# Optimization experiments

Measured on AMD Instinct MI355X. Metric: run time of the kernel, lower is better.

Reference implementation:

```python
import jax, jax.numpy as jnp
import numpy as np

BLANK = 0
B, T, U = 4, 128, 64
EPROJS, EMBED, DUNITS, JOINT, ODIM = 512, 512, 1024, 512, 2048


def lstm_cell(x, h, c, W_ih, W_hh, b_ih, b_hh):
    # PyTorch LSTMCell: gates ordered (i, f, g, o)
    gates = x @ W_ih.T + b_ih + h @ W_hh.T + b_hh
    i, f, g, o = jnp.split(gates, 4, axis=-1)
    c_new = jax.nn.sigmoid(f) * c + jax.nn.sigmoid(i) * jnp.tanh(g)
    h_new = jax.nn.sigmoid(o) * jnp.tanh(c_new)
    return h_new, c_new


def setup_inputs() -> dict:
    key = jax.random.key(0)
    ks = jax.random.split(key, 20)
    s = 0.05
    embed = jax.random.normal(ks[2], (ODIM, EMBED)) * s
    embed = embed.at[BLANK].set(0.0)  # padding_idx
    return {
        'hs_pad': jax.random.normal(ks[0], (B, T, EPROJS)),
        'ys_in_pad': jax.random.randint(ks[1], (B, U), 0, ODIM, dtype=jnp.int32),
        'embed': embed,
        'W_ih0': jax.random.normal(ks[3], (4 * DUNITS, EMBED)) * s,
        'W_hh0': jax.random.normal(ks[4], (4 * DUNITS, DUNITS)) * s,
        'b_ih0': jax.random.normal(ks[5], (4 * DUNITS,)) * s,
        'b_hh0': jax.random.normal(ks[6], (4 * DUNITS,)) * s,
        'W_ih1': jax.random.normal(ks[7], (4 * DUNITS, DUNITS)) * s,
        'W_hh1': jax.random.normal(ks[8], (4 * DUNITS, DUNITS)) * s,
        'b_ih1': jax.random.normal(ks[9], (4 * DUNITS,)) * s,
        'b_hh1': jax.random.normal(ks[10], (4 * DUNITS,)) * s,
        'W_enc': jax.random.normal(ks[11], (JOINT, EPROJS)) * s,
        'b_enc': jax.random.normal(ks[12], (JOINT,)) * s,
        'W_dec': jax.random.normal(ks[13], (JOINT, DUNITS)) * s,
        'W_out': jax.random.normal(ks[14], (ODIM, JOINT)) * s,
        'b_out': jax.random.normal(ks[15], (ODIM,)) * s,
    }


def reference(hs_pad, ys_in_pad, embed, W_ih0, W_hh0, b_ih0, b_hh0,
              W_ih1, W_hh1, b_ih1, b_hh1, W_enc, b_enc, W_dec, W_out, b_out):
    # Embedding with padding_idx=blank (blank row contributes zero).
    eys = embed[ys_in_pad] * (ys_in_pad != BLANK)[..., None].astype(embed.dtype)  # (B,U,E)

    def step(carry, ey):
        h0, c0, h1, c1 = carry
        h0, c0 = lstm_cell(ey, h0, c0, W_ih0, W_hh0, b_ih0, b_hh0)
        h1, c1 = lstm_cell(h0, h1, c1, W_ih1, W_hh1, b_ih1, b_hh1)
        return (h0, c0, h1, c1), h1

    z0 = jnp.zeros((hs_pad.shape[0], DUNITS), hs_pad.dtype)
    _, hs = jax.lax.scan(step, (z0, z0, z0, z0), jnp.swapaxes(eys, 0, 1))
    h_dec = jnp.swapaxes(hs, 0, 1)  # (B,U,Hdec)

    # Joint network: broadcast-add + tanh + output projection.
    enc_p = jnp.einsum('bte,je->btj', hs_pad, W_enc) + b_enc   # (B,T,J)
    dec_p = jnp.einsum('bud,jd->buj', h_dec, W_dec)            # (B,U,J)
    z = jnp.tanh(enc_p[:, :, None, :] + dec_p[:, None, :, :])  # (B,T,U,J)
    return jnp.einsum('btuj,oj->btuo', z, W_out) + b_out       # (B,T,U,odim)
```

## Files before the change

kernel.cpp:

```cpp
#include <hip/hip_runtime.h>
#include <stdint.h>

typedef short bf16x8 __attribute__((ext_vector_type(8)));
typedef float f32x4 __attribute__((ext_vector_type(4)));
typedef unsigned int u32x4 __attribute__((ext_vector_type(4)));

__device__ __forceinline__ unsigned short f2bf(float f) {
  union { float f; unsigned int i; } v; v.f = f;
  unsigned int r = v.i + 0x7FFF + ((v.i >> 16) & 1);
  return (unsigned short)(r >> 16);
}
__device__ __forceinline__ float bfu2f(unsigned short u) {
  union { unsigned int i; float f; } v; v.i = ((unsigned int)u) << 16; return v.f;
}
__device__ __forceinline__ void gload_lds16(const void* g, void* l) {
  __builtin_amdgcn_global_load_lds(
      (const __attribute__((address_space(1))) unsigned int*)g,
      (__attribute__((address_space(3))) unsigned int*)l,
      16, 0, 0);
}
__device__ __forceinline__ void store16_coh(unsigned int* p, u32x4 v) {
  asm volatile("global_store_dwordx4 %0, %1, off sc0 sc1" :: "v"(p), "v"(v) : "memory");
}
__device__ __forceinline__ void spin_load6(const unsigned int* p0, const unsigned int* p1,
                                           const unsigned int* p2, const unsigned int* p3,
                                           const unsigned int* p4, const unsigned int* p5,
                                           u32x4& r0, u32x4& r1, u32x4& r2,
                                           u32x4& r3, u32x4& r4, u32x4& r5) {
  asm volatile(
      "global_load_dwordx4 %0, %6, off sc0 sc1\n\t"
      "global_load_dwordx4 %1, %7, off sc0 sc1\n\t"
      "global_load_dwordx4 %2, %8, off sc0 sc1\n\t"
      "global_load_dwordx4 %3, %9, off sc0 sc1\n\t"
      "global_load_dwordx4 %4, %10, off sc0 sc1\n\t"
      "global_load_dwordx4 %5, %11, off sc0 sc1\n\t"
      "s_waitcnt vmcnt(0)"
      : "=&v"(r0), "=&v"(r1), "=&v"(r2), "=&v"(r3), "=&v"(r4), "=&v"(r5)
      : "v"(p0), "v"(p1), "v"(p2), "v"(p3), "v"(p4), "v"(p5)
      : "memory");
}
__device__ __forceinline__ void spin_load3p(const unsigned int* p0, const unsigned int* p1,
                                            const unsigned int* p2, const unsigned int* pp,
                                            u32x4& r0, u32x4& r1, u32x4& r2, unsigned int& pt) {
  asm volatile(
      "global_load_dwordx4 %0, %4, off sc0 sc1\n\t"
      "global_load_dwordx4 %1, %5, off sc0 sc1\n\t"
      "global_load_dwordx4 %2, %6, off sc0 sc1\n\t"
      "global_load_dword %3, %7, off sc0 sc1\n\t"
      "s_waitcnt vmcnt(0)"
      : "=&v"(r0), "=&v"(r1), "=&v"(r2), "=&v"(pt)
      : "v"(p0), "v"(p1), "v"(p2), "v"(pp)
      : "memory");
}

__global__ __launch_bounds__(256) void k_cvt(const float* __restrict__ s0, const float* __restrict__ s1,
                                             const float* __restrict__ s2, const float* __restrict__ s3,
                                             unsigned short* __restrict__ d0, unsigned short* __restrict__ d1,
                                             unsigned short* __restrict__ d2, unsigned short* __restrict__ d3) {
  int j = blockIdx.x * 256 + threadIdx.x;
  const float* s; unsigned short* d; int o;
  if (j < 524288)       { s = s0; d = d0; o = j; }
  else if (j < 1048576) { s = s1; d = d1; o = j - 524288; }
  else if (j < 1572864) { s = s2; d = d2; o = j - 1048576; }
  else                  { s = s3; d = d3; o = j - 1572864; }
  size_t off = (size_t)o * 8;
  f32x4 v0 = *(const f32x4*)(s + off);
  f32x4 v1 = *(const f32x4*)(s + off + 4);
  bf16x8 r;
#pragma unroll
  for (int k = 0; k < 4; k++) { r[k] = (short)f2bf(v0[k]); r[4 + k] = (short)f2bf(v1[k]); }
  *(bf16x8*)(d + off) = r;
}

__global__ __launch_bounds__(256) void k_prep(const int* __restrict__ ys,
                                              const float* __restrict__ embed,
                                              float* __restrict__ eys,
                                              unsigned int* __restrict__ exch) {
  int idx = blockIdx.x * 256 + threadIdx.x;
  int row = idx >> 6;
  int e = (idx & 63) * 8;
  int y = ys[row];
  f32x4 v0 = {0.f, 0.f, 0.f, 0.f}, v1 = {0.f, 0.f, 0.f, 0.f};
  if (y != 0) {
    v0 = *(const f32x4*)(embed + (size_t)y * 512 + e);
    v1 = *(const f32x4*)(embed + (size_t)y * 512 + e + 4);
  }
  *(f32x4*)(eys + (size_t)row * 512 + e) = v0;
  *(f32x4*)(eys + (size_t)row * 512 + e + 4) = v1;
  exch[idx] = 0u;
  exch[idx + 16384] = 0u;
}

__global__ __launch_bounds__(256) void k_gemm_bias(const float* __restrict__ A,
                                                   const float* __restrict__ W,
                                                   const float* __restrict__ b1,
                                                   const float* __restrict__ b2,
                                                   void* __restrict__ Cout, int obf,
                                                   int M, int N, int K) {
  __shared__ unsigned short Als[64][40];
  __shared__ unsigned short Wls[64][40];
  int tid = threadIdx.x;
  int lane = tid & 63, wid = tid >> 6;
  int mtiles = M >> 6;
  int mt = blockIdx.x % mtiles, nt = blockIdx.x / mtiles;
  int srow = tid >> 2, sseg = tid & 3;
  f32x4 acc[4];
#pragma unroll
  for (int nf = 0; nf < 4; nf++) acc[nf] = (f32x4){0.f, 0.f, 0.f, 0.f};

  for (int kc = 0; kc < K; kc += 32) {
    const float* ap = A + (size_t)(mt * 64 + srow) * K + kc + sseg * 8;
    const float* wp = W + (size_t)(nt * 64 + srow) * K + kc + sseg * 8;
    f32x4 a0 = *(const f32x4*)ap, a1 = *(const f32x4*)(ap + 4);
    f32x4 w0 = *(const f32x4*)wp, w1 = *(const f32x4*)(wp + 4);
    bf16x8 av, wv;
#pragma unroll
    for (int k = 0; k < 4; k++) {
      av[k] = (short)f2bf(a0[k]); av[4 + k] = (short)f2bf(a1[k]);
      wv[k] = (short)f2bf(w0[k]); wv[4 + k] = (short)f2bf(w1[k]);
    }
    __syncthreads();
    *(bf16x8*)(&Als[srow][sseg * 8]) = av;
    *(bf16x8*)(&Wls[srow][sseg * 8]) = wv;
    __syncthreads();
    bf16x8 af = *(const bf16x8*)(&Als[wid * 16 + (lane & 15)][(lane >> 4) * 8]);
#pragma unroll
    for (int nf = 0; nf < 4; nf++) {
      bf16x8 bf = *(const bf16x8*)(&Wls[nf * 16 + (lane & 15)][(lane >> 4) * 8]);
      acc[nf] = __builtin_amdgcn_mfma_f32_16x16x32_bf16(af, bf, acc[nf], 0, 0, 0);
    }
  }
  int rloc = (lane >> 4) * 4;
  int col0 = lane & 15;
#pragma unroll
  for (int nf = 0; nf < 4; nf++) {
    int n = nt * 64 + nf * 16 + col0;
    float bias = 0.f;
    if (b1) bias += b1[n];
    if (b2) bias += b2[n];
#pragma unroll
    for (int r = 0; r < 4; r++) {
      int m = mt * 64 + wid * 16 + rloc + r;
      float v = acc[nf][r] + bias;
      if (obf) ((unsigned short*)Cout)[(size_t)m * N + n] = f2bf(v);
      else     ((float*)Cout)[(size_t)m * N + n] = v;
    }
  }
}

__global__ __launch_bounds__(512) void k_lstm_fused(
    const float* __restrict__ X0,
    float* __restrict__ hdec,
    const unsigned short* __restrict__ W_hh0,
    const unsigned short* __restrict__ W_ih1,
    const unsigned short* __restrict__ W_hh1,
    const float* __restrict__ b_ih1,
    const float* __restrict__ b_hh1,
    unsigned int* __restrict__ exch) {
  __shared__ unsigned short X_lds[4][2064];
  __shared__ float red[8][4][16][4];
  int tid = threadIdx.x;
  int lane = tid & 63, w = tid >> 6;
  bool isL1 = blockIdx.x >= 64;
  int bidl = blockIdx.x & 63;
  int base = bidl * 16;
  unsigned int* REC0 = exch;
  unsigned int* REC1 = exch + 16384;

  bf16x8 wf[4][8];
  int ch = lane & 15;
  int klo = (lane >> 4) << 3;
  int kb = isL1 ? w * 256 : w * 128;
#pragma unroll
  for (int nt = 0; nt < 4; nt++) {
    int grow = nt * 1024 + base + ch;
    if (!isL1) {
#pragma unroll
      for (int ks = 0; ks < 4; ks++)
        wf[nt][ks] = *(const bf16x8*)(W_hh0 + (size_t)grow * 1024 + kb + ks * 32 + klo);
    } else {
#pragma unroll
      for (int ks = 0; ks < 8; ks++) {
        int k = kb + ks * 32 + klo;
        const unsigned short* src = (k < 1024) ? (W_ih1 + (size_t)grow * 1024 + k)
                                               : (W_hh1 + (size_t)grow * 1024 + (k - 1024));
        wf[nt][ks] = *(const bf16x8*)src;
      }
    }
  }

  float creg = 0.f;
  float bs0 = 0.f, bs1 = 0.f, bs2 = 0.f, bs3 = 0.f;
  int gch = tid >> 2, gb = tid & 3;
  if (isL1 && tid < 64) {
    int c = base + gch;
    bs0 = b_ih1[c] + b_hh1[c];
    bs1 = b_ih1[1024 + c] + b_hh1[1024 + c];
    bs2 = b_ih1[2048 + c] + b_hh1[2048 + c];
    bs3 = b_ih1[3072 + c] + b_hh1[3072 + c];
  }

  int uoff[3], upb[3], us[3]; bool uneed[3];
#pragma unroll
  for (int r = 0; r < 3; r++) {
    int u = tid + r * 512;
    uneed[r] = (u < 1408);
    int uc = uneed[r] ? u : 1407;
    int pb = uc / 22;
    int s = uc - pb * 22;
    upb[r] = pb; us[r] = s;
    uoff[r] = pb * 128 + s * 4;
  }

#define STAGE_UNIT(rv, rr, off1024)                                           \
  if (uneed[rv]) {                                                            \
    int pb_ = upb[rv], s_ = us[rv];                                           \
    _Pragma("unroll")                                                         \
    for (int j_ = 0; j_ < 3; j_++) {                                          \
      int i_ = 3 * s_ + j_;                                                   \
      if (i_ < 64) {                                                          \
        union { unsigned int u; float f; } cv_; cv_.u = rr[j_];               \
        X_lds[i_ & 3][off1024 + pb_ * 16 + (i_ >> 2)] = f2bf(cv_.f);          \
      }                                                                       \
    }                                                                         \
  }

  int ar = ch & 3;
  if (!isL1) {
    for (int p = 0; p < 64; p++) {
      float xp0 = 0.f, xp1 = 0.f, xp2 = 0.f, xp3 = 0.f;
      if (tid < 64) {
        const float* x0p = X0 + ((size_t)(gb * 64 + p)) * 4096 + base + gch;
        xp0 = x0p[0]; xp1 = x0p[1024]; xp2 = x0p[2048]; xp3 = x0p[3072];
      }
      {
        unsigned int* b0 = REC0 + (unsigned)(p & 1) * 8192;
        const unsigned int* pp = REC1 + (unsigned)((p - 1) & 1) * 8192 + (tid & 63) * 128 + 3;
        unsigned expP = (p == 0) ? 0u : (unsigned)(p - 1);
        u32x4 r0, r1, r2; unsigned int pt;
        while (true) {
          spin_load3p(b0 + uoff[0], b0 + uoff[1], b0 + uoff[2], pp, r0, r1, r2, pt);
          bool ok = (!uneed[0] || r0[3] == (unsigned)p) && (!uneed[1] || r1[3] == (unsigned)p) &&
                    (!uneed[2] || r2[3] == (unsigned)p) && (pt >= expP);
          if (ok) break;
          __builtin_amdgcn_s_sleep(1);
        }
        STAGE_UNIT(0, r0, 0) STAGE_UNIT(1, r1, 0) STAGE_UNIT(2, r2, 0)
      }
      __syncthreads();
      {
        f32x4 acc[4];
#pragma unroll
        for (int nt = 0; nt < 4; nt++) acc[nt] = (f32x4){0.f, 0.f, 0.f, 0.f};
#pragma unroll
        for (int ks = 0; ks < 4; ks++) {
          bf16x8 a = *(const bf16x8*)&X_lds[ar][kb + ks * 32 + klo];
#pragma unroll
          for (int nt = 0; nt < 4; nt++)
            acc[nt] = __builtin_amdgcn_mfma_f32_16x16x32_bf16(a, wf[nt][ks], acc[nt], 0, 0, 0);
        }
        if (lane < 16) {
#pragma unroll
          for (int nt = 0; nt < 4; nt++) *(f32x4*)&red[w][nt][lane][0] = acc[nt];
        }
      }
      __syncthreads();
      if (tid < 64) {
        float g0 = 0.f, g1 = 0.f, g2 = 0.f, g3 = 0.f;
#pragma unroll
        for (int w8 = 0; w8 < 8; w8++) {
          g0 += red[w8][0][gch][gb]; g1 += red[w8][1][gch][gb];
          g2 += red[w8][2][gch][gb]; g3 += red[w8][3][gch][gb];
        }
        g0 += xp0; g1 += xp1; g2 += xp2; g3 += xp3;
        float ii = 1.f / (1.f + __expf(-g0));
        float ff = 1.f / (1.f + __expf(-g1));
        float oo = 1.f / (1.f + __expf(-g3));
        float cn = ff * creg + ii * tanhf(g2);
        creg = cn;
        float hn = oo * tanhf(cn);
        int l = tid;
        float v0 = __shfl(hn, 3 * l);
        float v1 = __shfl(hn, 3 * l + 1);
        float v2 = __shfl(hn, 3 * l + 2);
        if (l < 22) {
          unsigned tag = (unsigned)(p + 1);
          unsigned int* rec = REC0 + (tag & 1) * 8192 + bidl * 128 + l * 4;
          u32x4 d;
          d[0] = __float_as_uint(v0); d[1] = __float_as_uint(v1);
          d[2] = __float_as_uint(v2); d[3] = tag;
          store16_coh(rec, d);
        }
      }
    }
  } else {
    for (int p = 1; p <= 64; p++) {
      {
        unsigned int* b0 = REC0 + (unsigned)(p & 1) * 8192;
        unsigned int* b1 = REC1 + (unsigned)((p - 1) & 1) * 8192;
        u32x4 r0, r1, r2, r3, r4, r5;
        unsigned exp0 = (unsigned)p, exp1 = (unsigned)(p - 1);
        while (true) {
          spin_load6(b0 + uoff[0], b0 + uoff[1], b0 + uoff[2],
                     b1 + uoff[0], b1 + uoff[1], b1 + uoff[2],
                     r0, r1, r2, r3, r4, r5);
          bool ok = (!uneed[0] || (r0[3] == exp0 && r3[3] == exp1)) &&
                    (!uneed[1] || (r1[3] == exp0 && r4[3] == exp1)) &&
                    (!uneed[2] || (r2[3] == exp0 && r5[3] == exp1));
          if (ok) break;
          __builtin_amdgcn_s_sleep(1);
        }
        STAGE_UNIT(0, r0, 0) STAGE_UNIT(1, r1, 0) STAGE_UNIT(2, r2, 0)
        STAGE_UNIT(0, r3, 1024) STAGE_UNIT(1, r4, 1024) STAGE_UNIT(2, r5, 1024)
      }
      __syncthreads();
      {
        f32x4 acc[4];
#pragma unroll
        for (int nt = 0; nt < 4; nt++) acc[nt] = (f32x4){0.f, 0.f, 0.f, 0.f};
#pragma unroll
        for (int ks = 0; ks < 8; ks++) {
          bf16x8 a = *(const bf16x8*)&X_lds[ar][kb + ks * 32 + klo];
#pragma unroll
          for (int nt = 0; nt < 4; nt++)
            acc[nt] = __builtin_amdgcn_mfma_f32_16x16x32_bf16(a, wf[nt][ks], acc[nt], 0, 0, 0);
        }
        if (lane < 16) {
#pragma unroll
          for (int nt = 0; nt < 4; nt++) *(f32x4*)&red[w][nt][lane][0] = acc[nt];
        }
      }
      __syncthreads();
      if (tid < 64) {
        float g0 = 0.f, g1 = 0.f, g2 = 0.f, g3 = 0.f;
#pragma unroll
        for (int w8 = 0; w8 < 8; w8++) {
          g0 += red[w8][0][gch][gb]; g1 += red[w8][1][gch][gb];
          g2 += red[w8][2][gch][gb]; g3 += red[w8][3][gch][gb];
        }
        g0 += bs0; g1 += bs1; g2 += bs2; g3 += bs3;
        float ii = 1.f / (1.f + __expf(-g0));
        float ff = 1.f / (1.f + __expf(-g1));
        float oo = 1.f / (1.f + __expf(-g3));
        float cn = ff * creg + ii * tanhf(g2);
        creg = cn;
        float hn = oo * tanhf(cn);
        hdec[((size_t)(gb * 64 + (p - 1))) * 1024 + base + gch] = hn;
        int l = tid;
        float v0 = __shfl(hn, 3 * l);
        float v1 = __shfl(hn, 3 * l + 1);
        float v2 = __shfl(hn, 3 * l + 2);
        if (l < 22) {
          unsigned tag = (unsigned)p;
          unsigned int* rec = REC1 + (tag & 1) * 8192 + bidl * 128 + l * 4;
          u32x4 d;
          d[0] = __float_as_uint(v0); d[1] = __float_as_uint(v1);
          d[2] = __float_as_uint(v2); d[3] = tag;
          store16_coh(rec, d);
        }
      }
    }
  }
#undef STAGE_UNIT
}

__global__ __launch_bounds__(256) void k_z(const unsigned short* __restrict__ encpb,
                                           const unsigned short* __restrict__ decpb,
                                           unsigned short* __restrict__ Z) {
  int idx = blockIdx.x * 256 + threadIdx.x;
  int m = idx >> 6;
  int k0 = (idx & 63) * 8;
  int bt = m >> 6;
  int b = m >> 13, u = m & 63;
  bf16x8 ev = *(const bf16x8*)(encpb + (size_t)bt * 512 + k0);
  bf16x8 dv = *(const bf16x8*)(decpb + (size_t)(b * 64 + u) * 512 + k0);
  bf16x8 r;
#pragma unroll
  for (int j = 0; j < 8; j++) {
    float x = bfu2f((unsigned short)ev[j]) + bfu2f((unsigned short)dv[j]);
    float e = __expf(x + x);
    r[j] = (short)f2bf(1.f - 2.f / (e + 1.f));
  }
  *(bf16x8*)(Z + (size_t)m * 512 + k0) = r;
}

__global__ __launch_bounds__(512, 2) void k_gemm_out(const unsigned short* __restrict__ Z,
                                                     const unsigned short* __restrict__ Wout,
                                                     const float* __restrict__ bout,
                                                     float* __restrict__ out) {
  __shared__ unsigned short Wls[8][8192];
  int tid = threadIdx.x;
  int lane = tid & 63, wid = tid >> 6;
  int bid = blockIdx.x;
  int mpart = bid & 15, ngroup = bid >> 4;

#pragma unroll
  for (int kc = 0; kc < 8; kc++) {
    unsigned short* dst = &Wls[kc][0];
#pragma unroll
    for (int q = 0; q < 2; q++) {
      int idx = tid + q * 512;
      int n = idx >> 3, sl = idx & 7;
      int ss = sl ^ (n & 7);
      gload_lds16(Wout + (size_t)(ngroup * 128 + n) * 512 + kc * 64 + ss * 8, dst + idx * 8);
    }
  }
  float bb[8];
#pragma unroll
  for (int nf = 0; nf < 8; nf++) bb[nf] = bout[ngroup * 128 + nf * 16 + (lane & 15)];
  asm volatile("s_waitcnt vmcnt(0)" ::: "memory");
  __syncthreads();

  int rowwave = mpart * 2048 + wid * 256;
  int ocol0 = ngroup * 128;
  for (int mg = 0; mg < 4; mg++) {
    int rowbase = rowwave + mg * 64;
    f32x4 acc[4][8];
#pragma unroll
    for (int mf = 0; mf < 4; mf++)
#pragma unroll
      for (int nf = 0; nf < 8; nf++) acc[mf][nf] = (f32x4){0.f, 0.f, 0.f, 0.f};

#pragma unroll
    for (int ks = 0; ks < 16; ks++) {
      bf16x8 a[4];
#pragma unroll
      for (int mf = 0; mf < 4; mf++) {
        int r = rowbase + mf * 16 + (lane & 15);
        a[mf] = *(const bf16x8*)(Z + (size_t)r * 512 + ks * 32 + ((lane >> 4) << 3));
      }
      const unsigned short* Wb = &Wls[ks >> 1][0];
      int slot = (ks & 1) * 4 + (lane >> 4);
#pragma unroll
      for (int nf = 0; nf < 8; nf++) {
        int nl = nf * 16 + (lane & 15);
        int phys = slot ^ (nl & 7);
        bf16x8 bfr = *(const bf16x8*)(Wb + nl * 64 + phys * 8);
#pragma unroll
        for (int mf = 0; mf < 4; mf++)
          acc[mf][nf] = __builtin_amdgcn_mfma_f32_16x16x32_bf16(a[mf], bfr, acc[mf][nf], 0, 0, 0);
      }
    }
#pragma unroll
    for (int mf = 0; mf < 4; mf++) {
      int rb = rowbase + mf * 16 + ((lane >> 4) << 2);
#pragma unroll
      for (int nf = 0; nf < 8; nf++) {
        int o = ocol0 + nf * 16 + (lane & 15);
        float bias = bb[nf];
#pragma unroll
        for (int q = 0; q < 4; q++)
          __builtin_nontemporal_store(acc[mf][nf][q] + bias, &out[(size_t)(rb + q) * 2048 + o]);
      }
    }
  }
}

extern "C" void kernel_launch(void* const* d_in, const int* in_sizes, int n_in,
                              void* d_out, int out_size, void* d_ws, size_t ws_size,
                              hipStream_t stream) {
  const float* hs   = (const float*)d_in[0];
  const int*   ys   = (const int*)d_in[1];
  const float* emb  = (const float*)d_in[2];
  const float* Wih0 = (const float*)d_in[3];
  const float* Whh0 = (const float*)d_in[4];
  const float* bih0 = (const float*)d_in[5];
  const float* bhh0 = (const float*)d_in[6];
  const float* Wih1 = (const float*)d_in[7];
  const float* Whh1 = (const float*)d_in[8];
  const float* bih1 = (const float*)d_in[9];
  const float* bhh1 = (const float*)d_in[10];
  const float* Wenc = (const float*)d_in[11];
  const float* benc = (const float*)d_in[12];
  const float* Wdec = (const float*)d_in[13];
  const float* Wout = (const float*)d_in[14];
  const float* bout = (const float*)d_in[15];

  char* ws = (char*)d_ws;
  unsigned short* Woutb = (unsigned short*)(ws + 0);
  unsigned short* encpb = (unsigned short*)(ws + 2097152);
  unsigned short* decpb = (unsigned short*)(ws + 2621440);
  unsigned int*   exch  = (unsigned int*)(ws + 2883584);
  unsigned short* Z     = (unsigned short*)(ws + 3031040);
  float*          eys   = (float*)(ws + 3031040);
  float*          X0    = (float*)(ws + 3555328);
  float*          hdec  = (float*)(ws + 7749632);
  unsigned short* Whh0b = (unsigned short*)(ws + 8798208);
  unsigned short* Wih1b = (unsigned short*)(ws + 17186816);
  unsigned short* Whh1b = (unsigned short*)(ws + 25575424);
  float*          out   = (float*)d_out;

  k_cvt<<<6656, 256, 0, stream>>>(Whh0, Wih1, Whh1, Wout, Whh0b, Wih1b, Whh1b, Woutb);
  k_prep<<<64, 256, 0, stream>>>(ys, emb, eys, exch);
  k_gemm_bias<<<256, 256, 0, stream>>>(eys, Wih0, bih0, bhh0, X0, 0, 256, 4096, 512);
  k_gemm_bias<<<64, 256, 0, stream>>>(hs, Wenc, benc, nullptr, encpb, 1, 512, 512, 512);
  k_lstm_fused<<<128, 512, 0, stream>>>(X0, hdec, Whh0b, Wih1b, Whh1b, bih1, bhh1, exch);
  k_gemm_bias<<<32, 256, 0, stream>>>(hdec, Wdec, nullptr, nullptr, decpb, 1, 256, 512, 1024);
  k_z<<<8192, 256, 0, stream>>>(encpb, decpb, Z);
  k_gemm_out<<<256, 512, 0, stream>>>(Z, Woutb, bout, out);
}
```

Before: 421.9 us.

## Fuse LSTM, decoder projection and joint GEMM into one persistent pipelined kernel

Merges the recurrent LSTM, the decoder projection, the tanh joint and the output GEMM into a single 256-block kernel. Decoder-projection blocks spin on the layer-1 hidden-state exchange and publish per-step tags. Joint blocks wait on those tags and compute each decoder step's output slice as soon as it is ready, building tanh(enc+dec) on the fly instead of materialising Z. The aim is to hide the joint GEMM behind the serial LSTM and remove the Z write/read and extra launches. This relies on all blocks being co-resident for the spin-waits and changes the output write order to a per-u stride.

```diff
diff --git a/kernel.cpp b/kernel.cpp
--- a/kernel.cpp
+++ b/kernel.cpp
@@ -55,14 +55,17 @@
 
 __global__ __launch_bounds__(256) void k_cvt(const float* __restrict__ s0, const float* __restrict__ s1,
                                              const float* __restrict__ s2, const float* __restrict__ s3,
+                                             const float* __restrict__ s4,
                                              unsigned short* __restrict__ d0, unsigned short* __restrict__ d1,
-                                             unsigned short* __restrict__ d2, unsigned short* __restrict__ d3) {
+                                             unsigned short* __restrict__ d2, unsigned short* __restrict__ d3,
+                                             unsigned short* __restrict__ d4) {
   int j = blockIdx.x * 256 + threadIdx.x;
   const float* s; unsigned short* d; int o;
   if (j < 524288)       { s = s0; d = d0; o = j; }
   else if (j < 1048576) { s = s1; d = d1; o = j - 524288; }
   else if (j < 1572864) { s = s2; d = d2; o = j - 1048576; }
-  else                  { s = s3; d = d3; o = j - 1572864; }
+  else if (j < 1703936) { s = s3; d = d3; o = j - 1572864; }
+  else                  { s = s4; d = d4; o = j - 1703936; }
   size_t off = (size_t)o * 8;
   f32x4 v0 = *(const f32x4*)(s + off);
   f32x4 v1 = *(const f32x4*)(s + off + 4);
@@ -75,7 +78,8 @@
 __global__ __launch_bounds__(256) void k_prep(const int* __restrict__ ys,
                                               const float* __restrict__ embed,
                                               float* __restrict__ eys,
-                                              unsigned int* __restrict__ exch) {
+                                              unsigned int* __restrict__ exch,
+                                              unsigned int* __restrict__ dtag) {
   int idx = blockIdx.x * 256 + threadIdx.x;
   int row = idx >> 6;
   int e = (idx & 63) * 8;
@@ -89,6 +93,7 @@
   *(f32x4*)(eys + (size_t)row * 512 + e + 4) = v1;
   exch[idx] = 0u;
   exch[idx + 16384] = 0u;
+  if (idx < 1024) dtag[idx] = 0u;
 }
 
 __global__ __launch_bounds__(256) void k_gemm_bias(const float* __restrict__ A,
@@ -148,100 +153,264 @@
   }
 }
 
-__global__ __launch_bounds__(512) void k_lstm_fused(
+__global__ __launch_bounds__(512) void k_mega(
     const float* __restrict__ X0,
-    float* __restrict__ hdec,
     const unsigned short* __restrict__ W_hh0,
     const unsigned short* __restrict__ W_ih1,
     const unsigned short* __restrict__ W_hh1,
     const float* __restrict__ b_ih1,
     const float* __restrict__ b_hh1,
-    unsigned int* __restrict__ exch) {
-  __shared__ unsigned short X_lds[4][2064];
-  __shared__ float red[8][4][16][4];
+    unsigned int* __restrict__ exch,
+    const unsigned short* __restrict__ Wdecb,
+    float* __restrict__ decpf,
+    unsigned int* __restrict__ dtag,
+    const unsigned short* __restrict__ encpb,
+    const unsigned short* __restrict__ Woutb,
+    const float* __restrict__ bout,
+    float* __restrict__ out) {
+  __shared__ unsigned long long smem[16384];
   int tid = threadIdx.x;
   int lane = tid & 63, w = tid >> 6;
-  bool isL1 = blockIdx.x >= 64;
-  int bidl = blockIdx.x & 63;
-  int base = bidl * 16;
+  int bid = blockIdx.x;
   unsigned int* REC0 = exch;
   unsigned int* REC1 = exch + 16384;
 
-  bf16x8 wf[4][8];
-  int ch = lane & 15;
-  int klo = (lane >> 4) << 3;
-  int kb = isL1 ? w * 256 : w * 128;
-#pragma unroll
-  for (int nt = 0; nt < 4; nt++) {
-    int grow = nt * 1024 + base + ch;
+  if (bid < 128) {
+    unsigned short (*X_lds)[2064] = (unsigned short (*)[2064])smem;
+    float (*red)[4][16][4] = (float (*)[4][16][4])((char*)smem + 16512);
+    bool isL1 = bid >= 64;
+    int bidl = bid & 63;
+    int base = bidl * 16;
+
+    bf16x8 wf[4][8];
+    int ch = lane & 15;
+    int klo = (lane >> 4) << 3;
+    int kb = isL1 ? w * 256 : w * 128;
+#pragma unroll
+    for (int nt = 0; nt < 4; nt++) {
+      int grow = nt * 1024 + base + ch;
+      if (!isL1) {
+#pragma unroll
+        for (int ks = 0; ks < 4; ks++)
+          wf[nt][ks] = *(const bf16x8*)(W_hh0 + (size_t)grow * 1024 + kb + ks * 32 + klo);
+      } else {
+#pragma unroll
+        for (int ks = 0; ks < 8; ks++) {
+          int k = kb + ks * 32 + klo;
+          const unsigned short* src = (k < 1024) ? (W_ih1 + (size_t)grow * 1024 + k)
+                                                 : (W_hh1 + (size_t)grow * 1024 + (k - 1024));
+          wf[nt][ks] = *(const bf16x8*)src;
+        }
+      }
+    }
+
+    float creg = 0.f;
+    float bs0 = 0.f, bs1 = 0.f, bs2 = 0.f, bs3 = 0.f;
+    int gch = tid >> 2, gb = tid & 3;
+    if (isL1 && tid < 64) {
+      int c = base + gch;
+      bs0 = b_ih1[c] + b_hh1[c];
+      bs1 = b_ih1[1024 + c] + b_hh1[1024 + c];
+      bs2 = b_ih1[2048 + c] + b_hh1[2048 + c];
+      bs3 = b_ih1[3072 + c] + b_hh1[3072 + c];
+    }
+
+    int uoff[3], upb[3], us[3]; bool uneed[3];
+#pragma unroll
+    for (int r = 0; r < 3; r++) {
+      int u = tid + r * 512;
+      uneed[r] = (u < 1408);
+      int uc = uneed[r] ? u : 1407;
+      int pb = uc / 22;
+      int s = uc - pb * 22;
+      upb[r] = pb; us[r] = s;
+      uoff[r] = pb * 128 + s * 4;
+    }
+
+#define STAGE_UNIT(rv, rr, off1024)                                           \
+    if (uneed[rv]) {                                                          \
+      int pb_ = upb[rv], s_ = us[rv];                                         \
+      _Pragma("unroll")                                                       \
+      for (int j_ = 0; j_ < 3; j_++) {                                        \
+        int i_ = 3 * s_ + j_;                                                 \
+        if (i_ < 64) {                                                        \
+          union { unsigned int u; float f; } cv_; cv_.u = rr[j_];             \
+          X_lds[i_ & 3][off1024 + pb_ * 16 + (i_ >> 2)] = f2bf(cv_.f);        \
+        }                                                                     \
+      }                                                                       \
+    }
+
+    int ar = ch & 3;
     if (!isL1) {
+      for (int p = 0; p < 64; p++) {
+        float xp0 = 0.f, xp1 = 0.f, xp2 = 0.f, xp3 = 0.f;
+        if (tid < 64) {
+          const float* x0p = X0 + ((size_t)(gb * 64 + p)) * 4096 + base + gch;
+          xp0 = x0p[0]; xp1 = x0p[1024]; xp2 = x0p[2048]; xp3 = x0p[3072];
+        }
+        {
+          unsigned int* b0 = REC0 + (unsigned)(p & 1) * 8192;
+          const unsigned int* pp = REC1 + (unsigned)((p - 1) & 1) * 8192 + (tid & 63) * 128 + 3;
+          unsigned expP = (p == 0) ? 0u : (unsigned)(p - 1);
+          u32x4 r0, r1, r2; unsigned int pt;
+          while (true) {
+            spin_load3p(b0 + uoff[0], b0 + uoff[1], b0 + uoff[2], pp, r0, r1, r2, pt);
+            bool ok = (!uneed[0] || r0[3] == (unsigned)p) && (!uneed[1] || r1[3] == (unsigned)p) &&
+                      (!uneed[2] || r2[3] == (unsigned)p) && (pt >= expP);
+            if (ok) break;
+            __builtin_amdgcn_s_sleep(1);
+          }
+          STAGE_UNIT(0, r0, 0) STAGE_UNIT(1, r1, 0) STAGE_UNIT(2, r2, 0)
+        }
+        __syncthreads();
+        {
+          f32x4 acc[4];
+#pragma unroll
+          for (int nt = 0; nt < 4; nt++) acc[nt] = (f32x4){0.f, 0.f, 0.f, 0.f};
+#pragma unroll
+          for (int ks = 0; ks < 4; ks++) {
+            bf16x8 a = *(const bf16x8*)&X_lds[ar][kb + ks * 32 + klo];
+#pragma unroll
+            for (int nt = 0; nt < 4; nt++)
+              acc[nt] = __builtin_amdgcn_mfma_f32_16x16x32_bf16(a, wf[nt][ks], acc[nt], 0, 0, 0);
+          }
+          if (lane < 16) {
+#pragma unroll
+            for (int nt = 0; nt < 4; nt++) *(f32x4*)&red[w][nt][lane][0] = acc[nt];
+          }
+        }
+        __syncthreads();
+        if (tid < 64) {
+          float g0 = 0.f, g1 = 0.f, g2 = 0.f, g3 = 0.f;
+#pragma unroll
+          for (int w8 = 0; w8 < 8; w8++) {
+            g0 += red[w8][0][gch][gb]; g1 += red[w8][1][gch][gb];
+            g2 += red[w8][2][gch][gb]; g3 += red[w8][3][gch][gb];
+          }
+          g0 += xp0; g1 += xp1; g2 += xp2; g3 += xp3;
+          float ii = 1.f / (1.f + __expf(-g0));
+          float ff = 1.f / (1.f + __expf(-g1));
+          float oo = 1.f / (1.f + __expf(-g3));
+          float cn = ff * creg + ii * tanhf(g2);
+          creg = cn;
+          float hn = oo * tanhf(cn);
+          int l = tid;
+          float v0 = __shfl(hn, 3 * l);
+          float v1 = __shfl(hn, 3 * l + 1);
+          float v2 = __shfl(hn, 3 * l + 2);
+          if (l < 22) {
+            unsigned tag = (unsigned)(p + 1);
+            unsigned int* rec = REC0 + (tag & 1) * 8192 + bidl * 128 + l * 4;
+            u32x4 d;
+            d[0] = __float_as_uint(v0); d[1] = __float_as_uint(v1);
+            d[2] = __float_as_uint(v2); d[3] = tag;
+            store16_coh(rec, d);
+          }
+        }
+      }
+    } else {
+      for (int p = 1; p <= 64; p++) {
+        {
+          unsigned int* b0 = REC0 + (unsigned)(p & 1) * 8192;
+          unsigned int* b1 = REC1 + (unsigned)((p - 1) & 1) * 8192;
+          u32x4 r0, r1, r2, r3, r4, r5;
+          unsigned exp0 = (unsigned)p, exp1 = (unsigned)(p - 1);
+          while (true) {
+            spin_load6(b0 + uoff[0], b0 + uoff[1], b0 + uoff[2],
+                       b1 + uoff[0], b1 + uoff[1], b1 + uoff[2],
+                       r0, r1, r2, r3, r4, r5);
+            bool ok = (!uneed[0] || (r0[3] == exp0 && r3[3] == exp1)) &&
+                      (!uneed[1] || (r1[3] == exp0 && r4[3] == exp1)) &&
+                      (!uneed[2] || (r2[3] == exp0 && r5[3] == exp1));
+            if (ok) break;
+            __builtin_amdgcn_s_sleep(1);
+          }
+          STAGE_UNIT(0, r0, 0) STAGE_UNIT(1, r1, 0) STAGE_UNIT(2, r2, 0)
+          STAGE_UNIT(0, r3, 1024) STAGE_UNIT(1, r4, 1024) STAGE_UNIT(2, r5, 1024)
+        }
+        __syncthreads();
+        {
+          f32x4 acc[4];
+#pragma unroll
+          for (int nt = 0; nt < 4; nt++) acc[nt] = (f32x4){0.f, 0.f, 0.f, 0.f};
+#pragma unroll
+          for (int ks = 0; ks < 8; ks++) {
+            bf16x8 a = *(const bf16x8*)&X_lds[ar][kb + ks * 32 + klo];
+#pragma unroll
+            for (int nt = 0; nt < 4; nt++)
+              acc[nt] = __builtin_amdgcn_mfma_f32_16x16x32_bf16(a, wf[nt][ks], acc[nt], 0, 0, 0);
+          }
+          if (lane < 16) {
+#pragma unroll
+            for (int nt = 0; nt < 4; nt++) *(f32x4*)&red[w][nt][lane][0] = acc[nt];
+          }
+        }
+        __syncthreads();
+        if (tid < 64) {
+          float g0 = 0.f, g1 = 0.f, g2 = 0.f, g3 = 0.f;
+#pragma unroll
+          for (int w8 = 0; w8 < 8; w8++) {
+            g0 += red[w8][0][gch][gb]; g1 += red[w8][1][gch][gb];
+            g2 += red[w8][2][gch][gb]; g3 += red[w8][3][gch][gb];
+          }
+          g0 += bs0; g1 += bs1; g2 += bs2; g3 += bs3;
+          float ii = 1.f / (1.f + __expf(-g0));
+          float ff = 1.f / (1.f + __expf(-g1));
+          float oo = 1.f / (1.f + __expf(-g3));
+          float cn = ff * creg + ii * tanhf(g2);
+          creg = cn;
+          float hn = oo * tanhf(cn);
+          int l = tid;
+          float v0 = __shfl(hn, 3 * l);
+          float v1 = __shfl(hn, 3 * l + 1);
+          float v2 = __shfl(hn, 3 * l + 2);
+          if (l < 22) {
+            unsigned tag = (unsigned)p;
+            unsigned int* rec = REC1 + (tag & 1) * 8192 + bidl * 128 + l * 4;
+            u32x4 d;
+            d[0] = __float_as_uint(v0); d[1] = __float_as_uint(v1);
+            d[2] = __float_as_uint(v2); d[3] = tag;
+            store16_coh(rec, d);
+          }
+        }
+      }
+    }
+  } else if (bid < 144) {
+    unsigned short (*X_lds)[2064] = (unsigned short (*)[2064])smem;
+    float (*red)[4][16][4] = (float (*)[4][16][4])((char*)smem + 16512);
+    int d = bid - 128;
+    int ch = lane & 15;
+    int klo = (lane >> 4) << 3;
+    int kb = w * 128;
+    bf16x8 wfd[2][4];
+#pragma unroll
+    for (int nt = 0; nt < 2; nt++) {
+      int grow = d * 32 + nt * 16 + ch;
 #pragma unroll
       for (int ks = 0; ks < 4; ks++)
-        wf[nt][ks] = *(const bf16x8*)(W_hh0 + (size_t)grow * 1024 + kb + ks * 32 + klo);
-    } else {
-#pragma unroll
-      for (int ks = 0; ks < 8; ks++) {
-        int k = kb + ks * 32 + klo;
-        const unsigned short* src = (k < 1024) ? (W_ih1 + (size_t)grow * 1024 + k)
-                                               : (W_hh1 + (size_t)grow * 1024 + (k - 1024));
-        wf[nt][ks] = *(const bf16x8*)src;
-      }
-    }
-  }
-
-  float creg = 0.f;
-  float bs0 = 0.f, bs1 = 0.f, bs2 = 0.f, bs3 = 0.f;
-  int gch = tid >> 2, gb = tid & 3;
-  if (isL1 && tid < 64) {
-    int c = base + gch;
-    bs0 = b_ih1[c] + b_hh1[c];
-    bs1 = b_ih1[1024 + c] + b_hh1[1024 + c];
-    bs2 = b_ih1[2048 + c] + b_hh1[2048 + c];
-    bs3 = b_ih1[3072 + c] + b_hh1[3072 + c];
-  }
-
-  int uoff[3], upb[3], us[3]; bool uneed[3];
-#pragma unroll
-  for (int r = 0; r < 3; r++) {
-    int u = tid + r * 512;
-    uneed[r] = (u < 1408);
-    int uc = uneed[r] ? u : 1407;
-    int pb = uc / 22;
-    int s = uc - pb * 22;
-    upb[r] = pb; us[r] = s;
-    uoff[r] = pb * 128 + s * 4;
-  }
-
-#define STAGE_UNIT(rv, rr, off1024)                                           \
-  if (uneed[rv]) {                                                            \
-    int pb_ = upb[rv], s_ = us[rv];                                           \
-    _Pragma("unroll")                                                         \
-    for (int j_ = 0; j_ < 3; j_++) {                                          \
-      int i_ = 3 * s_ + j_;                                                   \
-      if (i_ < 64) {                                                          \
-        union { unsigned int u; float f; } cv_; cv_.u = rr[j_];               \
-        X_lds[i_ & 3][off1024 + pb_ * 16 + (i_ >> 2)] = f2bf(cv_.f);          \
-      }                                                                       \
-    }                                                                         \
-  }
-
-  int ar = ch & 3;
-  if (!isL1) {
-    for (int p = 0; p < 64; p++) {
-      float xp0 = 0.f, xp1 = 0.f, xp2 = 0.f, xp3 = 0.f;
-      if (tid < 64) {
-        const float* x0p = X0 + ((size_t)(gb * 64 + p)) * 4096 + base + gch;
-        xp0 = x0p[0]; xp1 = x0p[1024]; xp2 = x0p[2048]; xp3 = x0p[3072];
-      }
+        wfd[nt][ks] = *(const bf16x8*)(Wdecb + (size_t)grow * 1024 + kb + ks * 32 + klo);
+    }
+    int uoff[3], upb[3], us[3]; bool uneed[3];
+#pragma unroll
+    for (int r = 0; r < 3; r++) {
+      int u = tid + r * 512;
+      uneed[r] = (u < 1408);
+      int uc = uneed[r] ? u : 1407;
+      int pb = uc / 22;
+      int s = uc - pb * 22;
+      upb[r] = pb; us[r] = s;
+      uoff[r] = pb * 128 + s * 4;
+    }
+    int ar = ch & 3;
+    for (int u = 0; u < 64; u++) {
+      unsigned expt = (unsigned)(u + 1);
       {
-        unsigned int* b0 = REC0 + (unsigned)(p & 1) * 8192;
-        const unsigned int* pp = REC1 + (unsigned)((p - 1) & 1) * 8192 + (tid & 63) * 128 + 3;
-        unsigned expP = (p == 0) ? 0u : (unsigned)(p - 1);
+        unsigned int* b1 = REC1 + (expt & 1) * 8192;
         u32x4 r0, r1, r2; unsigned int pt;
         while (true) {
-          spin_load3p(b0 + uoff[0], b0 + uoff[1], b0 + uoff[2], pp, r0, r1, r2, pt);
-          bool ok = (!uneed[0] || r0[3] == (unsigned)p) && (!uneed[1] || r1[3] == (unsigned)p) &&
-                    (!uneed[2] || r2[3] == (unsigned)p) && (pt >= expP);
+          spin_load3p(b1 + uoff[0], b1 + uoff[1], b1 + uoff[2], b1 + uoff[0] + 3, r0, r1, r2, pt);
+          bool ok = (!uneed[0] || r0[3] == expt) && (!uneed[1] || r1[3] == expt) &&
+                    (!uneed[2] || r2[3] == expt);
           if (ok) break;
           __builtin_amdgcn_s_sleep(1);
         }
@@ -249,211 +418,125 @@
       }
       __syncthreads();
       {
-        f32x4 acc[4];
-#pragma unroll
-        for (int nt = 0; nt < 4; nt++) acc[nt] = (f32x4){0.f, 0.f, 0.f, 0.f};
+        f32x4 acc[2];
+#pragma unroll
+        for (int nt = 0; nt < 2; nt++) acc[nt] = (f32x4){0.f, 0.f, 0.f, 0.f};
 #pragma unroll
         for (int ks = 0; ks < 4; ks++) {
           bf16x8 a = *(const bf16x8*)&X_lds[ar][kb + ks * 32 + klo];
 #pragma unroll
-          for (int nt = 0; nt < 4; nt++)
-            acc[nt] = __builtin_amdgcn_mfma_f32_16x16x32_bf16(a, wf[nt][ks], acc[nt], 0, 0, 0);
+          for (int nt = 0; nt < 2; nt++)
+            acc[nt] = __builtin_amdgcn_mfma_f32_16x16x32_bf16(a, wfd[nt][ks], acc[nt], 0, 0, 0);
         }
         if (lane < 16) {
 #pragma unroll
-          for (int nt = 0; nt < 4; nt++) *(f32x4*)&red[w][nt][lane][0] = acc[nt];
+          for (int nt = 0; nt < 2; nt++) *(f32x4*)&red[w][nt][lane][0] = acc[nt];
         }
       }
       __syncthreads();
-      if (tid < 64) {
-        float g0 = 0.f, g1 = 0.f, g2 = 0.f, g3 = 0.f;
-#pragma unroll
-        for (int w8 = 0; w8 < 8; w8++) {
-          g0 += red[w8][0][gch][gb]; g1 += red[w8][1][gch][gb];
-          g2 += red[w8][2][gch][gb]; g3 += red[w8][3][gch][gb];
-        }
-        g0 += xp0; g1 += xp1; g2 += xp2; g3 += xp3;
-        float ii = 1.f / (1.f + __expf(-g0));
-        float ff = 1.f / (1.f + __expf(-g1));
-        float oo = 1.f / (1.f + __expf(-g3));
-        float cn = ff * creg + ii * tanhf(g2);
-        creg = cn;
-        float hn = oo * tanhf(cn);
-        int l = tid;
-        float v0 = __shfl(hn, 3 * l);
-        float v1 = __shfl(hn, 3 * l + 1);
-        float v2 = __shfl(hn, 3 * l + 2);
-        if (l < 22) {
-          unsigned tag = (unsigned)(p + 1);
-          unsigned int* rec = REC0 + (tag & 1) * 8192 + bidl * 128 + l * 4;
-          u32x4 d;
-          d[0] = __float_as_uint(v0); d[1] = __float_as_uint(v1);
-          d[2] = __float_as_uint(v2); d[3] = tag;
-          store16_coh(rec, d);
-        }
-      }
+      if (tid < 128) {
+        int nt = tid >> 6, c = (tid >> 2) & 15, b = tid & 3;
+        float s = 0.f;
+#pragma unroll
+        for (int w8 = 0; w8 < 8; w8++) s += red[w8][nt][c][b];
+        __hip_atomic_store(&decpf[((size_t)(b * 64 + u)) * 512 + d * 32 + nt * 16 + c], s,
+                           __ATOMIC_RELAXED, __HIP_MEMORY_SCOPE_AGENT);
+      }
+      asm volatile("s_waitcnt vmcnt(0)" ::: "memory");
+      __syncthreads();
+      if (tid == 0)
+        __hip_atomic_store(&dtag[u * 16 + d], 1u, __ATOMIC_RELAXED, __HIP_MEMORY_SCOPE_AGENT);
+      __syncthreads();
     }
   } else {
-    for (int p = 1; p <= 64; p++) {
-      {
-        unsigned int* b0 = REC0 + (unsigned)(p & 1) * 8192;
-        unsigned int* b1 = REC1 + (unsigned)((p - 1) & 1) * 8192;
-        u32x4 r0, r1, r2, r3, r4, r5;
-        unsigned exp0 = (unsigned)p, exp1 = (unsigned)(p - 1);
-        while (true) {
-          spin_load6(b0 + uoff[0], b0 + uoff[1], b0 + uoff[2],
-                     b1 + uoff[0], b1 + uoff[1], b1 + uoff[2],
-                     r0, r1, r2, r3, r4, r5);
-          bool ok = (!uneed[0] || (r0[3] == exp0 && r3[3] == exp1)) &&
-                    (!uneed[1] || (r1[3] == exp0 && r4[3] == exp1)) &&
-                    (!uneed[2] || (r2[3] == exp0 && r5[3] == exp1));
-          if (ok) break;
-          __builtin_amdgcn_s_sleep(1);
-        }
-        STAGE_UNIT(0, r0, 0) STAGE_UNIT(1, r1, 0) STAGE_UNIT(2, r2, 0)
-        STAGE_UNIT(0, r3, 1024) STAGE_UNIT(1, r4, 1024) STAGE_UNIT(2, r5, 1024)
-      }
-      __syncthreads();
-      {
-        f32x4 acc[4];
-#pragma unroll
-        for (int nt = 0; nt < 4; nt++) acc[nt] = (f32x4){0.f, 0.f, 0.f, 0.f};
-#pragma unroll
-        for (int ks = 0; ks < 8; ks++) {
-          bf16x8 a = *(const bf16x8*)&X_lds[ar][kb + ks * 32 + klo];
-#pragma unroll
-          for (int nt = 0; nt < 4; nt++)
-            acc[nt] = __builtin_amdgcn_mfma_f32_16x16x32_bf16(a, wf[nt][ks], acc[nt], 0, 0, 0);
-        }
-        if (lane < 16) {
-#pragma unroll
-          for (int nt = 0; nt < 4; nt++) *(f32x4*)&red[w][nt][lane][0] = acc[nt];
-        }
-      }
-      __syncthreads();
-      if (tid < 64) {
-        float g0 = 0.f, g1 = 0.f, g2 = 0.f, g3 = 0.f;
-#pragma unroll
-        for (int w8 = 0; w8 < 8; w8++) {
-          g0 += red[w8][0][gch][gb]; g1 += red[w8][1][gch][gb];
-          g2 += red[w8][2][gch][gb]; g3 += red[w8][3][gch][gb];
-        }
-        g0 += bs0; g1 += bs1; g2 += bs2; g3 += bs3;
-        float ii = 1.f / (1.f + __expf(-g0));
-        float ff = 1.f / (1.f + __expf(-g1));
-        float oo = 1.f / (1.f + __expf(-g3));
-        float cn = ff * creg + ii * tanhf(g2);
-        creg = cn;
-        float hn = oo * tanhf(cn);
-        hdec[((size_t)(gb * 64 + (p - 1))) * 1024 + base + gch] = hn;
-        int l = tid;
-        float v0 = __shfl(hn, 3 * l);
-        float v1 = __shfl(hn, 3 * l + 1);
-        float v2 = __shfl(hn, 3 * l + 2);
-        if (l < 22) {
-          unsigned tag = (unsigned)p;
-          unsigned int* rec = REC1 + (tag & 1) * 8192 + bidl * 128 + l * 4;
-          u32x4 d;
-          d[0] = __float_as_uint(v0); d[1] = __float_as_uint(v1);
-          d[2] = __float_as_uint(v2); d[3] = tag;
-          store16_coh(rec, d);
+    unsigned short (*Wls)[8192] = (unsigned short (*)[8192])smem;
+    int jid = bid - 144;
+    int g = jid / 7, r = jid % 7;
+#pragma unroll
+    for (int kc = 0; kc < 8; kc++) {
+      unsigned short* dst = &Wls[kc][0];
+#pragma unroll
+      for (int q = 0; q < 2; q++) {
+        int idx = tid + q * 512;
+        int n = idx >> 3, sl = idx & 7;
+        int ss = sl ^ (n & 7);
+        gload_lds16(Woutb + (size_t)(g * 128 + n) * 512 + kc * 64 + ss * 8, dst + idx * 8);
+      }
+    }
+    float bb[8];
+#pragma unroll
+    for (int nf = 0; nf < 8; nf++) bb[nf] = bout[g * 128 + nf * 16 + (lane & 15)];
+    asm volatile("s_waitcnt vmcnt(0)" ::: "memory");
+    __syncthreads();
+
+    for (int u = r; u < 64; u += 7) {
+      while (true) {
+        unsigned t = 1u;
+        if (lane < 16)
+          t = __hip_atomic_load(&dtag[u * 16 + lane], __ATOMIC_RELAXED, __HIP_MEMORY_SCOPE_AGENT);
+        if (__all(t == 1u)) break;
+        __builtin_amdgcn_s_sleep(8);
+      }
+      f32x4 acc[4][8];
+#pragma unroll
+      for (int mf = 0; mf < 4; mf++)
+#pragma unroll
+        for (int nf = 0; nf < 8; nf++) acc[mf][nf] = (f32x4){0.f, 0.f, 0.f, 0.f};
+#pragma unroll
+      for (int ks = 0; ks < 16; ks++) {
+        int k0 = ks * 32 + ((lane >> 4) << 3);
+        bf16x8 a[4];
+#pragma unroll
+        for (int mf = 0; mf < 4; mf++) {
+          int row = w * 64 + mf * 16 + (lane & 15);
+          int b = row >> 7;
+          bf16x8 ev = *(const bf16x8*)(encpb + (size_t)row * 512 + k0);
+          const float* dp = decpf + ((size_t)(b * 64 + u)) * 512 + k0;
+          f32x4 d0 = *(const f32x4*)dp;
+          f32x4 d1 = *(const f32x4*)(dp + 4);
+          bf16x8 v;
+#pragma unroll
+          for (int j = 0; j < 4; j++) {
+            float x = bfu2f((unsigned short)ev[j]) + d0[j];
+            float e = __expf(x + x);
+            v[j] = (short)f2bf(1.f - 2.f / (e + 1.f));
+          }
+#pragma unroll
+          for (int j = 0; j < 4; j++) {
+            float x = bfu2f((unsigned short)ev[4 + j]) + d1[j];
+            float e = __expf(x + x);
+            v[4 + j] = (short)f2bf(1.f - 2.f / (e + 1.f));
+          }
+          a[mf] = v;
+        }
+        const unsigned short* Wb = &Wls[ks >> 1][0];
+        int slot = (ks & 1) * 4 + (lane >> 4);
+#pragma unroll
+        for (int nf = 0; nf < 8; nf++) {
+          int nl = nf * 16 + (lane & 15);
+          int phys = slot ^ (nl & 7);
+          bf16x8 bfr = *(const bf16x8*)(Wb + nl * 64 + phys * 8);
+#pragma unroll
+          for (int mf = 0; mf < 4; mf++)
+            acc[mf][nf] = __builtin_amdgcn_mfma_f32_16x16x32_bf16(a[mf], bfr, acc[mf][nf], 0, 0, 0);
+        }
+      }
+#pragma unroll
+      for (int mf = 0; mf < 4; mf++) {
+        int rb = w * 64 + mf * 16 + ((lane >> 4) << 2);
+#pragma unroll
+        for (int nf = 0; nf < 8; nf++) {
+          int o = g * 128 + nf * 16 + (lane & 15);
+          float bias = bb[nf];
+#pragma unroll
+          for (int q = 0; q < 4; q++)
+            __builtin_nontemporal_store(acc[mf][nf][q] + bias,
+                                        &out[((size_t)(rb + q) * 64 + u) * 2048 + o]);
         }
       }
     }
   }
 #undef STAGE_UNIT
-}
-
-__global__ __launch_bounds__(256) void k_z(const unsigned short* __restrict__ encpb,
-                                           const unsigned short* __restrict__ decpb,
-                                           unsigned short* __restrict__ Z) {
-  int idx = blockIdx.x * 256 + threadIdx.x;
-  int m = idx >> 6;
-  int k0 = (idx & 63) * 8;
-  int bt = m >> 6;
-  int b = m >> 13, u = m & 63;
-  bf16x8 ev = *(const bf16x8*)(encpb + (size_t)bt * 512 + k0);
-  bf16x8 dv = *(const bf16x8*)(decpb + (size_t)(b * 64 + u) * 512 + k0);
-  bf16x8 r;
-#pragma unroll
-  for (int j = 0; j < 8; j++) {
-    float x = bfu2f((unsigned short)ev[j]) + bfu2f((unsigned short)dv[j]);
-    float e = __expf(x + x);
-    r[j] = (short)f2bf(1.f - 2.f / (e + 1.f));
-  }
-  *(bf16x8*)(Z + (size_t)m * 512 + k0) = r;
-}
-
-__global__ __launch_bounds__(512, 2) void k_gemm_out(const unsigned short* __restrict__ Z,
-                                                     const unsigned short* __restrict__ Wout,
-                                                     const float* __restrict__ bout,
-                                                     float* __restrict__ out) {
-  __shared__ unsigned short Wls[8][8192];
-  int tid = threadIdx.x;
-  int lane = tid & 63, wid = tid >> 6;
-  int bid = blockIdx.x;
-  int mpart = bid & 15, ngroup = bid >> 4;
-
-#pragma unroll
-  for (int kc = 0; kc < 8; kc++) {
-    unsigned short* dst = &Wls[kc][0];
-#pragma unroll
-    for (int q = 0; q < 2; q++) {
-      int idx = tid + q * 512;
-      int n = idx >> 3, sl = idx & 7;
-      int ss = sl ^ (n & 7);
-      gload_lds16(Wout + (size_t)(ngroup * 128 + n) * 512 + kc * 64 + ss * 8, dst + idx * 8);
-    }
-  }
-  float bb[8];
-#pragma unroll
-  for (int nf = 0; nf < 8; nf++) bb[nf] = bout[ngroup * 128 + nf * 16 + (lane & 15)];
-  asm volatile("s_waitcnt vmcnt(0)" ::: "memory");
-  __syncthreads();
-
-  int rowwave = mpart * 2048 + wid * 256;
-  int ocol0 = ngroup * 128;
-  for (int mg = 0; mg < 4; mg++) {
-    int rowbase = rowwave + mg * 64;
-    f32x4 acc[4][8];
-#pragma unroll
-    for (int mf = 0; mf < 4; mf++)
-#pragma unroll
-      for (int nf = 0; nf < 8; nf++) acc[mf][nf] = (f32x4){0.f, 0.f, 0.f, 0.f};
-
-#pragma unroll
-    for (int ks = 0; ks < 16; ks++) {
-      bf16x8 a[4];
-#pragma unroll
-      for (int mf = 0; mf < 4; mf++) {
-        int r = rowbase + mf * 16 + (lane & 15);
-        a[mf] = *(const bf16x8*)(Z + (size_t)r * 512 + ks * 32 + ((lane >> 4) << 3));
-      }
-      const unsigned short* Wb = &Wls[ks >> 1][0];
-      int slot = (ks & 1) * 4 + (lane >> 4);
-#pragma unroll
-      for (int nf = 0; nf < 8; nf++) {
-        int nl = nf * 16 + (lane & 15);
-        int phys = slot ^ (nl & 7);
-        bf16x8 bfr = *(const bf16x8*)(Wb + nl * 64 + phys * 8);
-#pragma unroll
-        for (int mf = 0; mf < 4; mf++)
-          acc[mf][nf] = __builtin_amdgcn_mfma_f32_16x16x32_bf16(a[mf], bfr, acc[mf][nf], 0, 0, 0);
-      }
-    }
-#pragma unroll
-    for (int mf = 0; mf < 4; mf++) {
-      int rb = rowbase + mf * 16 + ((lane >> 4) << 2);
-#pragma unroll
-      for (int nf = 0; nf < 8; nf++) {
-        int o = ocol0 + nf * 16 + (lane & 15);
-        float bias = bb[nf];
-#pragma unroll
-        for (int q = 0; q < 4; q++)
-          __builtin_nontemporal_store(acc[mf][nf][q] + bias, &out[(size_t)(rb + q) * 2048 + o]);
-      }
-    }
-  }
 }
 
 extern "C" void kernel_launch(void* const* d_in, const int* in_sizes, int n_in,
@@ -478,24 +561,23 @@
 
   char* ws = (char*)d_ws;
   unsigned short* Woutb = (unsigned short*)(ws + 0);
-  unsigned short* encpb = (unsigned short*)(ws + 2097152);
-  unsigned short* decpb = (unsigned short*)(ws + 2621440);
-  unsigned int*   exch  = (unsigned int*)(ws + 2883584);
-  unsigned short* Z     = (unsigned short*)(ws + 3031040);
-  float*          eys   = (float*)(ws + 3031040);
-  float*          X0    = (float*)(ws + 3555328);
-  float*          hdec  = (float*)(ws + 7749632);
-  unsigned short* Whh0b = (unsigned short*)(ws + 8798208);
-  unsigned short* Wih1b = (unsigned short*)(ws + 17186816);
-  unsigned short* Whh1b = (unsigned short*)(ws + 25575424);
+  unsigned short* Wdecb = (unsigned short*)(ws + 2097152);
+  unsigned short* encpb = (unsigned short*)(ws + 3145728);
+  unsigned int*   exch  = (unsigned int*)(ws + 3670016);
+  unsigned int*   dtag  = (unsigned int*)(ws + 3801088);
+  float*          decpf = (float*)(ws + 3805184);
+  float*          eys   = (float*)(ws + 4329472);
+  float*          X0    = (float*)(ws + 4853760);
+  unsigned short* Whh0b = (unsigned short*)(ws + 9048064);
+  unsigned short* Wih1b = (unsigned short*)(ws + 17436672);
+  unsigned short* Whh1b = (unsigned short*)(ws + 25825280);
   float*          out   = (float*)d_out;
 
-  k_cvt<<<6656, 256, 0, stream>>>(Whh0, Wih1, Whh1, Wout, Whh0b, Wih1b, Whh1b, Woutb);
-  k_prep<<<64, 256, 0, stream>>>(ys, emb, eys, exch);
+  k_cvt<<<6912, 256, 0, stream>>>(Whh0, Wih1, Whh1, Wout, Wdec,
+                                  Whh0b, Wih1b, Whh1b, Woutb, Wdecb);
+  k_prep<<<64, 256, 0, stream>>>(ys, emb, eys, exch, dtag);
   k_gemm_bias<<<256, 256, 0, stream>>>(eys, Wih0, bih0, bhh0, X0, 0, 256, 4096, 512);
   k_gemm_bias<<<64, 256, 0, stream>>>(hs, Wenc, benc, nullptr, encpb, 1, 512, 512, 512);
-  k_lstm_fused<<<128, 512, 0, stream>>>(X0, hdec, Whh0b, Wih1b, Whh1b, bih1, bhh1, exch);
-  k_gemm_bias<<<32, 256, 0, stream>>>(hdec, Wdec, nullptr, nullptr, decpb, 1, 256, 512, 1024);
-  k_z<<<8192, 256, 0, stream>>>(encpb, decpb, Z);
-  k_gemm_out<<<256, 512, 0, stream>>>(Z, Woutb, bout, out);
-}
+  k_mega<<<256, 512, 0, stream>>>(X0, Whh0b, Wih1b, Whh1b, bih1, bhh1, exch,
+                                  Wdecb, decpf, dtag, encpb, Woutb, bout, out);
+}
```

Measured after the change: 1.260 ms. 199% more time.
